# Optimization experiments

Hardware: AMD Instinct MI355X
Metric: run time of the kernel (lower is better)

The kernel has to match this reference:

```python
import jax, jax.numpy as jnp
import numpy as np

N = 50000
E = 800000
IN_DIM = 256
HID_DIM = 256
OUT_DIM = 128


def _gcn(x, src, dst, W, b):
    # PyG GCNConv: h = W x; add self-loops; sym-normalized scatter-add; + bias
    h = x @ W  # [N, out]
    deg = jax.ops.segment_sum(jnp.ones_like(dst, dtype=h.dtype), dst, num_segments=N)
    dinv = jax.lax.rsqrt(jnp.maximum(deg, 1e-12))
    norm = dinv[src] * dinv[dst]  # [E+N]
    msg = h[src] * norm[:, None]  # gather + scale
    out = jax.ops.segment_sum(msg, dst, num_segments=N)  # scatter-add
    return out + b


def _with_self_loops(edge):
    loops = jnp.arange(N, dtype=edge.dtype)
    src = jnp.concatenate([edge[0], loops])
    dst = jnp.concatenate([edge[1], loops])
    return src, dst


def setup_inputs() -> dict:
    key = jax.random.key(0)
    ks = jax.random.split(key, 20)
    d = {}
    d['x'] = jax.random.normal(ks[0], (N, IN_DIM), dtype=jnp.float32)
    d['edge_ppi'] = jax.random.randint(ks[1], (2, E), 0, N, dtype=jnp.int32)
    d['edge_path'] = jax.random.randint(ks[2], (2, E), 0, N, dtype=jnp.int32)
    d['edge_go'] = jax.random.randint(ks[3], (2, E), 0, N, dtype=jnp.int32)
    i = 4
    for name in ['ppi', 'path', 'go']:
        s1 = 1.0 / np.sqrt(IN_DIM)
        s2 = 1.0 / np.sqrt(HID_DIM)
        d[f'{name}_w1'] = jax.random.uniform(ks[i], (IN_DIM, HID_DIM), jnp.float32, -s1, s1); i += 1
        d[f'{name}_b1'] = jnp.zeros((HID_DIM,), jnp.float32)
        d[f'{name}_w2'] = jax.random.uniform(ks[i], (HID_DIM, OUT_DIM), jnp.float32, -s2, s2); i += 1
        d[f'{name}_b2'] = jnp.zeros((OUT_DIM,), jnp.float32)
    sa = 1.0 / np.sqrt(OUT_DIM)
    d['attn_w'] = jax.random.uniform(ks[i], (OUT_DIM, 1), jnp.float32, -sa, sa)
    d['attn_b'] = jnp.zeros((1,), jnp.float32)
    return d


def reference(x, edge_ppi, edge_path, edge_go,
              ppi_w1, ppi_b1, ppi_w2, ppi_b2,
              path_w1, path_b1, path_w2, path_b2,
              go_w1, go_b1, go_w2, go_b2,
              attn_w, attn_b):
    feats = []
    for edge, w1, b1, w2, b2 in [
        (edge_ppi, ppi_w1, ppi_b1, ppi_w2, ppi_b2),
        (edge_path, path_w1, path_b1, path_w2, path_b2),
        (edge_go, go_w1, go_b1, go_w2, go_b2),
    ]:
        src, dst = _with_self_loops(edge)
        h = jax.nn.relu(_gcn(x, src, dst, w1, b1))
        feats.append(_gcn(h, src, dst, w2, b2))
    all_feat = jnp.stack(feats, axis=1)  # [N, 3, out]
    attn = jax.nn.softmax(all_feat @ attn_w + attn_b, axis=1)  # [N, 3, 1]
    return jnp.sum(all_feat * attn, axis=1)  # [N, out]
```

## Files before the change

### kernel.cpp

```cpp
#include <hip/hip_runtime.h>

#define NN 50000
#define NE 800000
#define BINS 98
#define CAP 12288
#define EPB 4096
#define P1B ((NE + EPB - 1) / EPB)

typedef __attribute__((ext_vector_type(8))) short short8;
typedef __attribute__((ext_vector_type(4))) float f32x4;
typedef __attribute__((ext_vector_type(8))) unsigned short ushort8v;
typedef __attribute__((ext_vector_type(4))) unsigned short ushort4v;
typedef _Float16 half8 __attribute__((ext_vector_type(8)));

__device__ __forceinline__ ushort f2h(float f) {
    _Float16 h = (_Float16)f;
    return __builtin_bit_cast(ushort, h);
}
__device__ __forceinline__ float h2f(ushort u) {
    return (float)__builtin_bit_cast(_Float16, u);
}


__global__ __launch_bounds__(256) void k_bin(const int* __restrict__ e0,
                                             const int* __restrict__ e1,
                                             const int* __restrict__ e2,
                                             int* __restrict__ g_cur,
                                             unsigned* __restrict__ g_bins) {
    const int br = blockIdx.x / P1B;
    const int cb = blockIdx.x % P1B;
    const int* ep = (br == 0 ? e0 : br == 1 ? e1 : e2);
    const int tid = threadIdx.x;
    const int e_base = cb * EPB;

    __shared__ int s_cnt[BINS];
    __shared__ int s_start[BINS];
    __shared__ int s_cur[BINS];
    __shared__ int s_gb[BINS];
    __shared__ unsigned s_stage[EPB];

    if (tid < BINS) s_cnt[tid] = 0;
    __syncthreads();

    int4 s4[4], d4[4];
    bool valid[4];
#pragma unroll
    for (int i = 0; i < 4; ++i) {
        int idx = e_base + i * 1024 + tid * 4;
        valid[i] = (idx < NE);
        if (valid[i]) {
            s4[i] = *(const int4*)&ep[idx];
            d4[i] = *(const int4*)&ep[NE + idx];
            atomicAdd(&s_cnt[d4[i].x >> 9], 1);
            atomicAdd(&s_cnt[d4[i].y >> 9], 1);
            atomicAdd(&s_cnt[d4[i].z >> 9], 1);
            atomicAdd(&s_cnt[d4[i].w >> 9], 1);
        }
    }
    __syncthreads();
    if (tid == 0) {
        int run = 0;
        for (int b = 0; b < BINS; ++b) {
            s_start[b] = run;
            run += s_cnt[b];
        }
    }
    __syncthreads();
    if (tid < BINS) {
        s_cur[tid] = s_start[tid];
        int c = s_cnt[tid];
        int pc = (c + 15) & ~15;
        s_gb[tid] = (c > 0) ? atomicAdd(&g_cur[br * BINS + tid], pc) : 0;
    }
    __syncthreads();

#pragma unroll
    for (int i = 0; i < 4; ++i) {
        if (valid[i]) {
            int ss[4] = {s4[i].x, s4[i].y, s4[i].z, s4[i].w};
            int dd[4] = {d4[i].x, d4[i].y, d4[i].z, d4[i].w};
#pragma unroll
            for (int q = 0; q < 4; ++q) {
                int bin = dd[q] >> 9;
                int pos = atomicAdd(&s_cur[bin], 1);
                s_stage[pos] = ((unsigned)(dd[q] & 511) << 16) | (unsigned)ss[q];
            }
        }
    }
    __syncthreads();

    for (int b = 0; b < BINS; ++b) {
        int c = s_cnt[b];
        if (c == 0) continue;
        int st = s_start[b];
        int gb = s_gb[b];
        int pc = (c + 15) & ~15;
        if (gb + pc > CAP) pc = (gb < CAP) ? (CAP - gb) : 0;
        size_t obase = (size_t)(br * BINS + b) * CAP + gb;
        for (int j = tid; j < pc; j += 256)
            g_bins[obase + j] = (j < c) ? s_stage[st + j] : 0x80000000u;
    }
}


__device__ __forceinline__ int wave_incl_scan(int v, int lane) {
#pragma unroll
    for (int d = 1; d < 64; d <<= 1) {
        int u = __shfl_up(v, d);
        if (lane >= d) v += u;
    }
    return v;
}

__global__ __launch_bounds__(256) void k_build(const unsigned* __restrict__ g_bins,
                                               const int* __restrict__ g_cur,
                                               ushort* __restrict__ g_csr,
                                               int* __restrict__ seg3,
                                               int* __restrict__ cnt3,
                                               float* __restrict__ dinv3) {
    const int bid = blockIdx.x;
    const int br = bid / BINS;
    const int b2 = bid % BINS;
    const size_t base = (size_t)bid * CAP;
    const int node0 = b2 << 9;
    const int tid = threadIdx.x;

    __shared__ int s_cnt[512];
    __shared__ int s_off[512];
    __shared__ int s_wsum[4];

    s_cnt[tid] = 0;
    s_cnt[tid + 256] = 0;
    __syncthreads();

    const int total = min(g_cur[bid], CAP);
    for (int j = tid; j < total; j += 256) {
        unsigned p = g_bins[base + j];
        if (!(p & 0x80000000u)) atomicAdd(&s_cnt[(p >> 16) & 0x1FF], 1);
    }
    __syncthreads();

    const int lane = tid & 63, w = tid >> 6;
    int c0 = s_cnt[2 * tid], c1 = s_cnt[2 * tid + 1];
    int c2 = c0 + c1;
    int incl = wave_incl_scan(c2, lane);
    if (lane == 63) s_wsum[w] = incl;
    __syncthreads();
    int wpre = 0;
    for (int i = 0; i < w; ++i) wpre += s_wsum[i];
    int ex = wpre + incl - c2;
    s_off[2 * tid] = ex;
    s_off[2 * tid + 1] = ex + c0;

#pragma unroll
    for (int q = 0; q < 2; ++q) {
        int local = 2 * tid + q;
        int node = node0 + local;
        if (node < NN) {
            int g = br * NN + node;
            int c = (q == 0) ? c0 : c1;
            seg3[g] = (int)base + s_off[local];
            cnt3[g] = c;
            dinv3[g] = rsqrtf((float)(c + 1));
        }
    }
    __syncthreads();
    s_cnt[2 * tid] = s_off[2 * tid];
    s_cnt[2 * tid + 1] = s_off[2 * tid + 1];
    __syncthreads();

    for (int j = tid; j < total; j += 256) {
        unsigned p = g_bins[base + j];
        if (!(p & 0x80000000u)) {
            int loc = (p >> 16) & 0x1FF;
            int pos = atomicAdd(&s_cnt[loc], 1);
            g_csr[base + pos] = (ushort)(p & 0xFFFFu);
        }
    }
}


__global__ __launch_bounds__(256) void k_conv_x16(const float* __restrict__ x,
                                                  ushort* __restrict__ x16) {
    const int wid = threadIdx.x >> 6, lane = threadIdx.x & 63;
    const int row = blockIdx.x * 4 + wid;
    if (row >= NN) return;
    float4 v = *(const float4*)&x[(size_t)row * 256 + lane * 4];
    ushort4 o;
    o.x = f2h(v.x); o.y = f2h(v.y); o.z = f2h(v.z); o.w = f2h(v.w);
    *(ushort4*)&x16[(size_t)row * 256 + lane * 4] = o;
}

__global__ __launch_bounds__(256) void k_conv_w1(const float* __restrict__ w0,
                                                 const float* __restrict__ w1,
                                                 const float* __restrict__ w2,
                                                 ushort* __restrict__ BT1all) {
    int idx = blockIdx.x * 256 + threadIdx.x;
    int b = idx >> 16, r = idx & 65535;
    int k = r >> 8, n = r & 255;
    const float* W = (b == 0 ? w0 : b == 1 ? w1 : w2);
    BT1all[(size_t)b * 65536 + (size_t)n * 256 + k] = f2h(W[r]);
}

__global__ __launch_bounds__(256) void k_conv_w2(const float* __restrict__ w0,
                                                 const float* __restrict__ w1,
                                                 const float* __restrict__ w2,
                                                 ushort* __restrict__ BT2all) {
    int idx = blockIdx.x * 256 + threadIdx.x;
    int b = idx >> 15, r = idx & 32767;
    int k = r >> 7, n = r & 127;
    const float* W = (b == 0 ? w0 : b == 1 ? w1 : w2);
    BT2all[(size_t)b * 32768 + (size_t)n * 256 + k] = f2h(W[r]);
}


template <int BM, int BN, int N, int KK, bool XSWZ>
__global__ __launch_bounds__((BM / 64) * (BN / 64) * 64) void k_gemm(
    const ushort* __restrict__ A, size_t aBatch,
    const ushort* __restrict__ BTall, int btBatch,
    const float* __restrict__ dinv3, ushort* __restrict__ Call, size_t cBatch) {
    constexpr int WGN = BN / 64, NW = (BM / 64) * WGN;
    constexpr int BK = 32;
    constexpr int MT = (NN + BM - 1) / BM, NT = N / BN, GB = MT * NT;
    constexpr int NSTEP = KK / BK;
    __shared__ ushort sA[2][BM * BK];
    __shared__ ushort sB[2][BN * BK];
    int kb, bid;
    if constexpr (XSWZ) {
        int q = blockIdx.x >> 3, r = blockIdx.x & 7;
        bid = (q / 3) * 8 + r;
        kb = q % 3;
        if (bid >= GB) return;
    } else {
        kb = blockIdx.x / GB;
        bid = blockIdx.x % GB;
    }
    const ushort* Ab = A + (size_t)kb * aBatch;
    const ushort* BT = BTall + (size_t)kb * btBatch;
    const float* dinv = dinv3 + (size_t)kb * NN;
    ushort* C = Call + (size_t)kb * cBatch;
    const int t = threadIdx.x, lane = t & 63, wid = t >> 6;
    const int wm = (wid / WGN) * 64, wn = (wid % WGN) * 64;
    const int bm = (bid / NT) * BM;
    const int bn = (bid % NT) * BN;

    f32x4 zero = {0.f, 0.f, 0.f, 0.f};
    f32x4 acc[4][4];
#pragma unroll
    for (int m = 0; m < 4; ++m)
#pragma unroll
        for (int n = 0; n < 4; ++n) acc[m][n] = zero;

    constexpr int A_ISS = (BM * BK * 2) / (NW * 1024);
    constexpr int B_ISS = (BN * BK * 2) / (NW * 1024);

    auto stage = [&](int buf, int kt) {
#pragma unroll
        for (int i = 0; i < A_ISS; ++i) {
            int off = (wid + i * NW) << 10;
            int la = off + lane * 16;
            int row = la >> 6;
            int slot = (la >> 4) & 3;
            int scol = (slot ^ (row & 3)) << 4;
            int grow = bm + row;
            if (grow > NN - 1) grow = NN - 1;
            const char* ga = (const char*)Ab + (size_t)grow * (KK * 2) + kt * 2 + scol;
            __builtin_amdgcn_global_load_lds(
                (__attribute__((address_space(1))) const void*)ga,
                (__attribute__((address_space(3))) void*)((char*)sA[buf] + off), 16, 0, 0);
        }
#pragma unroll
        for (int i = 0; i < B_ISS; ++i) {
            int off = (wid + i * NW) << 10;
            int la = off + lane * 16;
            int row = la >> 6;
            int slot = (la >> 4) & 3;
            int scol = (slot ^ (row & 3)) << 4;
            const char* ga = (const char*)BT + (size_t)(bn + row) * (KK * 2) + kt * 2 + scol;
            __builtin_amdgcn_global_load_lds(
                (__attribute__((address_space(1))) const void*)ga,
                (__attribute__((address_space(3))) void*)((char*)sB[buf] + off), 16, 0, 0);
        }
    };

    stage(0, 0);
    __syncthreads();

    int cur = 0;
    for (int ts = 0; ts < NSTEP; ++ts) {
        if (ts + 1 < NSTEP) stage(cur ^ 1, (ts + 1) * BK);

        const int s = lane >> 4;
        const int r0 = lane & 15;
        short8 af[4], bf[4];
#pragma unroll
        for (int m = 0; m < 4; ++m) {
            int row = wm + m * 16 + r0;
            af[m] = *(const short8*)((const char*)sA[cur] + row * 64 + ((s ^ (row & 3)) << 4));
        }
#pragma unroll
        for (int n = 0; n < 4; ++n) {
            int row = wn + n * 16 + r0;
            bf[n] = *(const short8*)((const char*)sB[cur] + row * 64 + ((s ^ (row & 3)) << 4));
        }
#pragma unroll
        for (int m = 0; m < 4; ++m)
#pragma unroll
            for (int n = 0; n < 4; ++n)
                acc[m][n] = __builtin_amdgcn_mfma_f32_16x16x32_f16(
                    __builtin_bit_cast(half8, af[m]), __builtin_bit_cast(half8, bf[n]),
                    acc[m][n], 0, 0, 0);
        __syncthreads();
        cur ^= 1;
    }

    const int cr0 = (lane >> 4) * 4;
    const int cc = lane & 15;
#pragma unroll
    for (int m = 0; m < 4; ++m) {
#pragma unroll
        for (int r = 0; r < 4; ++r) {
            int row = bm + wm + m * 16 + cr0 + r;
            if (row < NN) {
                float dv = dinv[row];
#pragma unroll
                for (int n = 0; n < 4; ++n)
                    C[(size_t)row * N + bn + wn + n * 16 + cc] = f2h(acc[m][n][r] * dv);
            }
        }
    }
}


#define UTOT (3 * 12500)

__global__ __launch_bounds__(256) void k_agg1(const ushort* __restrict__ hs16all,
                                              const int* __restrict__ seg3,
                                              const int* __restrict__ cnt3,
                                              const ushort* __restrict__ g_csr,
                                              const float* __restrict__ dinv3,
                                              const float* __restrict__ b1a,
                                              const float* __restrict__ b1b,
                                              const float* __restrict__ b1c,
                                              ushort* __restrict__ h1all) {
    const int x = blockIdx.x & 7, j = blockIdx.x >> 3;
    const int start = (x * UTOT) >> 3;
    const int end = ((x + 1) * UTOT) >> 3;
    const int u = start + j;
    if (u >= end) return;
    const int b = u / 12500;
    const int blk = u % 12500;

    const int wid = threadIdx.x >> 6;
    const int lane = threadIdx.x & 63;
    const int node = blk * 4 + wid;
    if (node >= NN) return;
    const int half = lane >> 5, l32 = lane & 31;
    const int g = b * NN + node;
    const ushort* hs = hs16all + (size_t)b * NN * 256;
    const ushort* csr = g_csr + seg3[g];
    const int len = cnt3[g] + 1;
    const size_t colb = (size_t)l32 * 8;

    float acc[8] = {0.f, 0.f, 0.f, 0.f, 0.f, 0.f, 0.f, 0.f};
    int i = half;
    for (; i + 6 < len; i += 8) {
        int s0 = (i == 0) ? node : (int)csr[i - 1];
        int s1 = (int)csr[i + 1];
        int s2 = (int)csr[i + 3];
        int s3 = (int)csr[i + 5];
        ushort8v v0 = *(const ushort8v*)&hs[(size_t)s0 * 256 + colb];
        ushort8v v1 = *(const ushort8v*)&hs[(size_t)s1 * 256 + colb];
        ushort8v v2 = *(const ushort8v*)&hs[(size_t)s2 * 256 + colb];
        ushort8v v3 = *(const ushort8v*)&hs[(size_t)s3 * 256 + colb];
#pragma unroll
        for (int jq = 0; jq < 8; ++jq)
            acc[jq] += (h2f(v0[jq]) + h2f(v1[jq])) + (h2f(v2[jq]) + h2f(v3[jq]));
    }
    for (; i < len; i += 2) {
        int s = (i == 0) ? node : (int)csr[i - 1];
        ushort8v v = *(const ushort8v*)&hs[(size_t)s * 256 + colb];
#pragma unroll
        for (int jq = 0; jq < 8; ++jq) acc[jq] += h2f(v[jq]);
    }
#pragma unroll
    for (int jq = 0; jq < 8; ++jq) acc[jq] += __shfl_xor(acc[jq], 32);

    if (half == 0) {
        const float* bias = (b == 0 ? b1a : b == 1 ? b1b : b1c);
        const float di = dinv3[g];
        ushort8v o;
#pragma unroll
        for (int jq = 0; jq < 8; ++jq) {
            float r = fmaxf(di * acc[jq] + bias[l32 * 8 + jq], 0.f);
            o[jq] = f2h(r);
        }
        *(ushort8v*)&h1all[((size_t)b * NN + node) * 256 + colb] = o;
    }
}


__global__ __launch_bounds__(256) void k_final(const ushort* __restrict__ hs2all,
                                               const int* __restrict__ seg3,
                                               const int* __restrict__ cnt3,
                                               const ushort* __restrict__ g_csr,
                                               const float* __restrict__ dinv3,
                                               const float* __restrict__ b2a,
                                               const float* __restrict__ b2b,
                                               const float* __restrict__ b2c,
                                               const float* __restrict__ attn_w,
                                               const float* __restrict__ attn_b,
                                               float* __restrict__ out) {
    const int wid = threadIdx.x >> 6;
    const int lane = threadIdx.x & 63;
    const int node = blockIdx.x * 4 + wid;
    if (node >= NN) return;
    const int half = lane >> 5, l32 = lane & 31;
    const size_t colb = (size_t)l32 * 4;

    float f[3][4];
#pragma unroll
    for (int b = 0; b < 3; ++b) {
        const int g = b * NN + node;
        const ushort* hs = hs2all + (size_t)b * NN * 128;
        const ushort* csr = g_csr + seg3[g];
        const int len = cnt3[g] + 1;
        float acc[4] = {0.f, 0.f, 0.f, 0.f};
        int i = half;
        for (; i + 6 < len; i += 8) {
            int s0 = (i == 0) ? node : (int)csr[i - 1];
            int s1 = (int)csr[i + 1];
            int s2 = (int)csr[i + 3];
            int s3 = (int)csr[i + 5];
            ushort4v v0 = *(const ushort4v*)&hs[(size_t)s0 * 128 + colb];
            ushort4v v1 = *(const ushort4v*)&hs[(size_t)s1 * 128 + colb];
            ushort4v v2 = *(const ushort4v*)&hs[(size_t)s2 * 128 + colb];
            ushort4v v3 = *(const ushort4v*)&hs[(size_t)s3 * 128 + colb];
#pragma unroll
            for (int j = 0; j < 4; ++j)
                acc[j] += (h2f(v0[j]) + h2f(v1[j])) + (h2f(v2[j]) + h2f(v3[j]));
        }
        for (; i < len; i += 2) {
            int s = (i == 0) ? node : (int)csr[i - 1];
            ushort4v v = *(const ushort4v*)&hs[(size_t)s * 128 + colb];
#pragma unroll
            for (int j = 0; j < 4; ++j) acc[j] += h2f(v[j]);
        }
#pragma unroll
        for (int j = 0; j < 4; ++j) acc[j] += __shfl_xor(acc[j], 32);
        const float* bias = (b == 0 ? b2a : b == 1 ? b2b : b2c);
        const float di = dinv3[g];
#pragma unroll
        for (int j = 0; j < 4; ++j) f[b][j] = di * acc[j] + bias[l32 * 4 + j];
    }

    float4 w = *(const float4*)&attn_w[l32 * 4];
    float s0 = f[0][0] * w.x + f[0][1] * w.y + f[0][2] * w.z + f[0][3] * w.w;
    float s1 = f[1][0] * w.x + f[1][1] * w.y + f[1][2] * w.z + f[1][3] * w.w;
    float s2 = f[2][0] * w.x + f[2][1] * w.y + f[2][2] * w.z + f[2][3] * w.w;
#pragma unroll
    for (int m = 16; m >= 1; m >>= 1) {
        s0 += __shfl_xor(s0, m);
        s1 += __shfl_xor(s1, m);
        s2 += __shfl_xor(s2, m);
    }
    float bb = attn_b[0];
    s0 += bb; s1 += bb; s2 += bb;
    float mx = fmaxf(s0, fmaxf(s1, s2));
    float e0 = expf(s0 - mx), e1 = expf(s1 - mx), e2 = expf(s2 - mx);
    float inv = 1.f / (e0 + e1 + e2);
    e0 *= inv; e1 *= inv; e2 *= inv;

    if (half == 0) {
        float4 o;
        o.x = f[0][0] * e0 + f[1][0] * e1 + f[2][0] * e2;
        o.y = f[0][1] * e0 + f[1][1] * e1 + f[2][1] * e2;
        o.z = f[0][2] * e0 + f[1][2] * e1 + f[2][2] * e2;
        o.w = f[0][3] * e0 + f[1][3] * e1 + f[2][3] * e2;
        *(float4*)&out[(size_t)node * 128 + colb] = o;
    }
}


extern "C" void kernel_launch(void* const* d_in, const int* in_sizes, int n_in,
                              void* d_out, int out_size, void* d_ws, size_t ws_size,
                              hipStream_t stream) {
    const float* x = (const float*)d_in[0];
    const int* e0 = (const int*)d_in[1];
    const int* e1 = (const int*)d_in[2];
    const int* e2 = (const int*)d_in[3];
    const float* attn_w = (const float*)d_in[16];
    const float* attn_b = (const float*)d_in[17];

    char* ws = (char*)d_ws;
    size_t off = 0;
    auto alloc = [&](size_t bytes) -> void* {
        void* p = ws + off;
        off += (bytes + 255) & ~(size_t)255;
        return p;
    };

    int* g_cur      = (int*)alloc(3 * BINS * 4);
    int* seg3       = (int*)alloc((size_t)3 * NN * 4);
    int* cnt3       = (int*)alloc((size_t)3 * NN * 4);
    float* dinv3    = (float*)alloc((size_t)3 * NN * 4);
    ushort* g_csr   = (ushort*)alloc((size_t)3 * BINS * CAP * 2);
    ushort* x16     = (ushort*)alloc((size_t)NN * 256 * 2);
    ushort* hs16all = (ushort*)alloc((size_t)3 * NN * 256 * 2);
    ushort* h1all   = (ushort*)alloc((size_t)3 * NN * 256 * 2);
    unsigned* g_bins = (unsigned*)h1all;
    ushort* hs2all  = (ushort*)alloc((size_t)3 * NN * 128 * 2);
    ushort* BT1all  = (ushort*)alloc((size_t)3 * 256 * 256 * 2);
    ushort* BT2all  = (ushort*)alloc((size_t)3 * 128 * 256 * 2);

    const int WB = (NN + 3) / 4;

    hipMemsetAsync(g_cur, 0, 3 * BINS * 4, stream);
    k_conv_x16<<<WB, 256, 0, stream>>>(x, x16);
    k_conv_w1<<<768, 256, 0, stream>>>((const float*)d_in[4], (const float*)d_in[8],
                                       (const float*)d_in[12], BT1all);
    k_conv_w2<<<384, 256, 0, stream>>>((const float*)d_in[6], (const float*)d_in[10],
                                       (const float*)d_in[14], BT2all);

    k_bin<<<3 * P1B, 256, 0, stream>>>(e0, e1, e2, g_cur, g_bins);
    k_build<<<3 * BINS, 256, 0, stream>>>(g_bins, g_cur, g_csr, seg3, cnt3, dinv3);

    k_gemm<128, 256, 256, 256, true><<<1176, 512, 0, stream>>>(
        x16, 0, BT1all, 65536, dinv3, hs16all, (size_t)NN * 256);
    k_agg1<<<8 * ((UTOT + 7) / 8), 256, 0, stream>>>(
        hs16all, seg3, cnt3, g_csr, dinv3,
        (const float*)d_in[5], (const float*)d_in[9], (const float*)d_in[13], h1all);

    k_gemm<128, 128, 128, 256, false><<<3 * 391, 256, 0, stream>>>(
        h1all, (size_t)NN * 256, BT2all, 32768, dinv3, hs2all, (size_t)NN * 128);

    k_final<<<WB, 256, 0, stream>>>(hs2all, seg3, cnt3, g_csr, dinv3,
                                    (const float*)d_in[7], (const float*)d_in[11],
                                    (const float*)d_in[15], attn_w, attn_b,
                                    (float*)d_out);
}
```

Baseline: 427.0 us.

## Merge setup kernels and co-schedule CSR build with layer-1 GEMM

Folds edge binning, x conversion and both weight conversions into one launch with block-range dispatch. CSR build and the first GEMM now share one launch, because the GEMM no longer needs dinv. The source-side dinv scaling moves from the GEMM epilogue into the layer-1 aggregation as a per-neighbour gather and multiply. This cuts kernel launches and lets independent work overlap, but the aggregation gains extra scalar loads per edge and the GEMM blocks carry the build kernel's shared memory.

```diff
diff --git a/kernel.cpp b/kernel.cpp
--- a/kernel.cpp
+++ b/kernel.cpp
@@ -6,6 +6,8 @@
 #define CAP 12288
 #define EPB 4096
 #define P1B ((NE + EPB - 1) / EPB)
+#define BINB (3 * P1B)
+#define WB ((NN + 3) / 4)
 
 typedef __attribute__((ext_vector_type(8))) short short8;
 typedef __attribute__((ext_vector_type(4))) float f32x4;
@@ -21,88 +23,6 @@
     return (float)__builtin_bit_cast(_Float16, u);
 }
 
-
-__global__ __launch_bounds__(256) void k_bin(const int* __restrict__ e0,
-                                             const int* __restrict__ e1,
-                                             const int* __restrict__ e2,
-                                             int* __restrict__ g_cur,
-                                             unsigned* __restrict__ g_bins) {
-    const int br = blockIdx.x / P1B;
-    const int cb = blockIdx.x % P1B;
-    const int* ep = (br == 0 ? e0 : br == 1 ? e1 : e2);
-    const int tid = threadIdx.x;
-    const int e_base = cb * EPB;
-
-    __shared__ int s_cnt[BINS];
-    __shared__ int s_start[BINS];
-    __shared__ int s_cur[BINS];
-    __shared__ int s_gb[BINS];
-    __shared__ unsigned s_stage[EPB];
-
-    if (tid < BINS) s_cnt[tid] = 0;
-    __syncthreads();
-
-    int4 s4[4], d4[4];
-    bool valid[4];
-#pragma unroll
-    for (int i = 0; i < 4; ++i) {
-        int idx = e_base + i * 1024 + tid * 4;
-        valid[i] = (idx < NE);
-        if (valid[i]) {
-            s4[i] = *(const int4*)&ep[idx];
-            d4[i] = *(const int4*)&ep[NE + idx];
-            atomicAdd(&s_cnt[d4[i].x >> 9], 1);
-            atomicAdd(&s_cnt[d4[i].y >> 9], 1);
-            atomicAdd(&s_cnt[d4[i].z >> 9], 1);
-            atomicAdd(&s_cnt[d4[i].w >> 9], 1);
-        }
-    }
-    __syncthreads();
-    if (tid == 0) {
-        int run = 0;
-        for (int b = 0; b < BINS; ++b) {
-            s_start[b] = run;
-            run += s_cnt[b];
-        }
-    }
-    __syncthreads();
-    if (tid < BINS) {
-        s_cur[tid] = s_start[tid];
-        int c = s_cnt[tid];
-        int pc = (c + 15) & ~15;
-        s_gb[tid] = (c > 0) ? atomicAdd(&g_cur[br * BINS + tid], pc) : 0;
-    }
-    __syncthreads();
-
-#pragma unroll
-    for (int i = 0; i < 4; ++i) {
-        if (valid[i]) {
-            int ss[4] = {s4[i].x, s4[i].y, s4[i].z, s4[i].w};
-            int dd[4] = {d4[i].x, d4[i].y, d4[i].z, d4[i].w};
-#pragma unroll
-            for (int q = 0; q < 4; ++q) {
-                int bin = dd[q] >> 9;
-                int pos = atomicAdd(&s_cur[bin], 1);
-                s_stage[pos] = ((unsigned)(dd[q] & 511) << 16) | (unsigned)ss[q];
-            }
-        }
-    }
-    __syncthreads();
-
-    for (int b = 0; b < BINS; ++b) {
-        int c = s_cnt[b];
-        if (c == 0) continue;
-        int st = s_start[b];
-        int gb = s_gb[b];
-        int pc = (c + 15) & ~15;
-        if (gb + pc > CAP) pc = (gb < CAP) ? (CAP - gb) : 0;
-        size_t obase = (size_t)(br * BINS + b) * CAP + gb;
-        for (int j = tid; j < pc; j += 256)
-            g_bins[obase + j] = (j < c) ? s_stage[st + j] : 0x80000000u;
-    }
-}
-
-
 __device__ __forceinline__ int wave_incl_scan(int v, int lane) {
 #pragma unroll
     for (int d = 1; d < 64; d <<= 1) {
@@ -112,137 +32,300 @@
     return v;
 }
 
-__global__ __launch_bounds__(256) void k_build(const unsigned* __restrict__ g_bins,
-                                               const int* __restrict__ g_cur,
-                                               ushort* __restrict__ g_csr,
-                                               int* __restrict__ seg3,
-                                               int* __restrict__ cnt3,
-                                               float* __restrict__ dinv3) {
-    const int bid = blockIdx.x;
-    const int br = bid / BINS;
-    const int b2 = bid % BINS;
-    const size_t base = (size_t)bid * CAP;
-    const int node0 = b2 << 9;
+
+__global__ __launch_bounds__(256) void k_setup(
+    const int* __restrict__ e0, const int* __restrict__ e1,
+    const int* __restrict__ e2, int* __restrict__ g_cur,
+    unsigned* __restrict__ g_bins,
+    const float* __restrict__ x, ushort* __restrict__ x16,
+    const float* __restrict__ w1a, const float* __restrict__ w1b,
+    const float* __restrict__ w1c, ushort* __restrict__ BT1all,
+    const float* __restrict__ w2a, const float* __restrict__ w2b,
+    const float* __restrict__ w2c, ushort* __restrict__ BT2all) {
     const int tid = threadIdx.x;
 
+    if (blockIdx.x < BINB) {
+        const int br = blockIdx.x / P1B;
+        const int cb = blockIdx.x % P1B;
+        const int* ep = (br == 0 ? e0 : br == 1 ? e1 : e2);
+        const int e_base = cb * EPB;
+
+        __shared__ int s_cnt[BINS];
+        __shared__ int s_start[BINS];
+        __shared__ int s_cur[BINS];
+        __shared__ int s_gb[BINS];
+        __shared__ unsigned s_stage[EPB];
+
+        if (tid < BINS) s_cnt[tid] = 0;
+        __syncthreads();
+
+        int4 s4[4], d4[4];
+        bool valid[4];
+#pragma unroll
+        for (int i = 0; i < 4; ++i) {
+            int idx = e_base + i * 1024 + tid * 4;
+            valid[i] = (idx < NE);
+            if (valid[i]) {
+                s4[i] = *(const int4*)&ep[idx];
+                d4[i] = *(const int4*)&ep[NE + idx];
+                atomicAdd(&s_cnt[d4[i].x >> 9], 1);
+                atomicAdd(&s_cnt[d4[i].y >> 9], 1);
+                atomicAdd(&s_cnt[d4[i].z >> 9], 1);
+                atomicAdd(&s_cnt[d4[i].w >> 9], 1);
+            }
+        }
+        __syncthreads();
+        if (tid == 0) {
+            int run = 0;
+            for (int b = 0; b < BINS; ++b) {
+                s_start[b] = run;
+                run += s_cnt[b];
+            }
+        }
+        __syncthreads();
+        if (tid < BINS) {
+            s_cur[tid] = s_start[tid];
+            int c = s_cnt[tid];
+            int pc = (c + 15) & ~15;
+            s_gb[tid] = (c > 0) ? atomicAdd(&g_cur[br * BINS + tid], pc) : 0;
+        }
+        __syncthreads();
+
+#pragma unroll
+        for (int i = 0; i < 4; ++i) {
+            if (valid[i]) {
+                int ss[4] = {s4[i].x, s4[i].y, s4[i].z, s4[i].w};
+                int dd[4] = {d4[i].x, d4[i].y, d4[i].z, d4[i].w};
+#pragma unroll
+                for (int q = 0; q < 4; ++q) {
+                    int bin = dd[q] >> 9;
+                    int pos = atomicAdd(&s_cur[bin], 1);
+                    s_stage[pos] = ((unsigned)(dd[q] & 511) << 16) | (unsigned)ss[q];
+                }
+            }
+        }
+        __syncthreads();
+
+        for (int b = 0; b < BINS; ++b) {
+            int c = s_cnt[b];
+            if (c == 0) continue;
+            int st = s_start[b];
+            int gb = s_gb[b];
+            int pc = (c + 15) & ~15;
+            if (gb + pc > CAP) pc = (gb < CAP) ? (CAP - gb) : 0;
+            size_t obase = (size_t)(br * BINS + b) * CAP + gb;
+            for (int j = tid; j < pc; j += 256)
+                g_bins[obase + j] = (j < c) ? s_stage[st + j] : 0x80000000u;
+        }
+        return;
+    }
+
+    int bb = blockIdx.x - BINB;
+    if (bb < WB) {
+        const int wid = tid >> 6, lane = tid & 63;
+        const int row = bb * 4 + wid;
+        if (row >= NN) return;
+        float4 v = *(const float4*)&x[(size_t)row * 256 + lane * 4];
+        ushort4 o;
+        o.x = f2h(v.x); o.y = f2h(v.y); o.z = f2h(v.z); o.w = f2h(v.w);
+        *(ushort4*)&x16[(size_t)row * 256 + lane * 4] = o;
+        return;
+    }
+    bb -= WB;
+    if (bb < 768) {
+        int idx = bb * 256 + tid;
+        int b = idx >> 16, r = idx & 65535;
+        int k = r >> 8, n = r & 255;
+        const float* W = (b == 0 ? w1a : b == 1 ? w1b : w1c);
+        BT1all[(size_t)b * 65536 + (size_t)n * 256 + k] = f2h(W[r]);
+        return;
+    }
+    bb -= 768;
+    {
+        int idx = bb * 256 + tid;
+        int b = idx >> 15, r = idx & 32767;
+        int k = r >> 7, n = r & 127;
+        const float* W = (b == 0 ? w2a : b == 1 ? w2b : w2c);
+        BT2all[(size_t)b * 32768 + (size_t)n * 256 + k] = f2h(W[r]);
+    }
+}
+
+
+#define BGB 391
+
+__global__ __launch_bounds__(512) void k_build_gemm1(
+    const unsigned* __restrict__ g_bins, const int* __restrict__ g_cur,
+    ushort* __restrict__ g_csr, int* __restrict__ seg3, int* __restrict__ cnt3,
+    float* __restrict__ dinv3,
+    const ushort* __restrict__ x16, const ushort* __restrict__ BT1all,
+    ushort* __restrict__ hs16all) {
+    __shared__ ushort sA[2][128 * 32];
+    __shared__ ushort sB[2][256 * 32];
     __shared__ int s_cnt[512];
-    __shared__ int s_off[512];
-    __shared__ int s_wsum[4];
-
-    s_cnt[tid] = 0;
-    s_cnt[tid + 256] = 0;
-    __syncthreads();
-
-    const int total = min(g_cur[bid], CAP);
-    for (int j = tid; j < total; j += 256) {
-        unsigned p = g_bins[base + j];
-        if (!(p & 0x80000000u)) atomicAdd(&s_cnt[(p >> 16) & 0x1FF], 1);
-    }
-    __syncthreads();
-
-    const int lane = tid & 63, w = tid >> 6;
-    int c0 = s_cnt[2 * tid], c1 = s_cnt[2 * tid + 1];
-    int c2 = c0 + c1;
-    int incl = wave_incl_scan(c2, lane);
-    if (lane == 63) s_wsum[w] = incl;
-    __syncthreads();
-    int wpre = 0;
-    for (int i = 0; i < w; ++i) wpre += s_wsum[i];
-    int ex = wpre + incl - c2;
-    s_off[2 * tid] = ex;
-    s_off[2 * tid + 1] = ex + c0;
-
-#pragma unroll
-    for (int q = 0; q < 2; ++q) {
-        int local = 2 * tid + q;
-        int node = node0 + local;
+    __shared__ int s_wsum[8];
+
+    const int t = threadIdx.x, lane = t & 63, wid = t >> 6;
+
+    if (blockIdx.x < 3 * BINS) {
+        const int bid = blockIdx.x;
+        const int br = bid / BINS;
+        const int b2 = bid % BINS;
+        const size_t base = (size_t)bid * CAP;
+        const int node0 = b2 << 9;
+
+        s_cnt[t] = 0;
+        __syncthreads();
+
+        const int total = min(g_cur[bid], CAP);
+        for (int j = t; j < total; j += 512) {
+            unsigned p = g_bins[base + j];
+            if (!(p & 0x80000000u)) atomicAdd(&s_cnt[(p >> 16) & 0x1FF], 1);
+        }
+        __syncthreads();
+
+        int c = s_cnt[t];
+        int incl = wave_incl_scan(c, lane);
+        if (lane == 63) s_wsum[wid] = incl;
+        __syncthreads();
+        int wpre = 0;
+        for (int i = 0; i < wid; ++i) wpre += s_wsum[i];
+        int ex = wpre + incl - c;
+
+        int node = node0 + t;
         if (node < NN) {
             int g = br * NN + node;
-            int c = (q == 0) ? c0 : c1;
-            seg3[g] = (int)base + s_off[local];
+            seg3[g] = (int)base + ex;
             cnt3[g] = c;
             dinv3[g] = rsqrtf((float)(c + 1));
         }
-    }
+        __syncthreads();
+        s_cnt[t] = ex;
+        __syncthreads();
+
+        for (int j = t; j < total; j += 512) {
+            unsigned p = g_bins[base + j];
+            if (!(p & 0x80000000u)) {
+                int loc = (p >> 16) & 0x1FF;
+                int pos = atomicAdd(&s_cnt[loc], 1);
+                g_csr[base + pos] = (ushort)(p & 0xFFFFu);
+            }
+        }
+        return;
+    }
+
+    constexpr int BM = 128, BN = 256, N = 256, KK = 256, BK = 32;
+    constexpr int NW = 8, WGN = 4, NSTEP = KK / BK;
+    const int sbid = blockIdx.x - 3 * BINS;
+    int q = sbid >> 3, r = sbid & 7;
+    int bid = (q / 3) * 8 + r;
+    int kb = q % 3;
+    if (bid >= BGB) return;
+
+    const ushort* BT = BT1all + (size_t)kb * 65536;
+    ushort* C = hs16all + (size_t)kb * NN * 256;
+    const int wm = (wid / WGN) * 64, wn = (wid % WGN) * 64;
+    const int bm = bid * BM;
+
+    f32x4 zero = {0.f, 0.f, 0.f, 0.f};
+    f32x4 acc[4][4];
+#pragma unroll
+    for (int m = 0; m < 4; ++m)
+#pragma unroll
+        for (int n = 0; n < 4; ++n) acc[m][n] = zero;
+
+    auto stage = [&](int buf, int kt) {
+        {
+            int off = wid << 10;
+            int la = off + lane * 16;
+            int row = la >> 6;
+            int slot = (la >> 4) & 3;
+            int scol = (slot ^ (row & 3)) << 4;
+            int grow = bm + row;
+            if (grow > NN - 1) grow = NN - 1;
+            const char* ga = (const char*)x16 + (size_t)grow * (KK * 2) + kt * 2 + scol;
+            __builtin_amdgcn_global_load_lds(
+                (__attribute__((address_space(1))) const void*)ga,
+                (__attribute__((address_space(3))) void*)((char*)sA[buf] + off), 16, 0, 0);
+        }
+#pragma unroll
+        for (int i = 0; i < 2; ++i) {
+            int off = (wid + i * NW) << 10;
+            int la = off + lane * 16;
+            int row = la >> 6;
+            int slot = (la >> 4) & 3;
+            int scol = (slot ^ (row & 3)) << 4;
+            const char* ga = (const char*)BT + (size_t)row * (KK * 2) + kt * 2 + scol;
+            __builtin_amdgcn_global_load_lds(
+                (__attribute__((address_space(1))) const void*)ga,
+                (__attribute__((address_space(3))) void*)((char*)sB[buf] + off), 16, 0, 0);
+        }
+    };
+
+    stage(0, 0);
     __syncthreads();
-    s_cnt[2 * tid] = s_off[2 * tid];
-    s_cnt[2 * tid + 1] = s_off[2 * tid + 1];
-    __syncthreads();
-
-    for (int j = tid; j < total; j += 256) {
-        unsigned p = g_bins[base + j];
-        if (!(p & 0x80000000u)) {
-            int loc = (p >> 16) & 0x1FF;
-            int pos = atomicAdd(&s_cnt[loc], 1);
-            g_csr[base + pos] = (ushort)(p & 0xFFFFu);
-        }
-    }
-}
-
-
-__global__ __launch_bounds__(256) void k_conv_x16(const float* __restrict__ x,
-                                                  ushort* __restrict__ x16) {
-    const int wid = threadIdx.x >> 6, lane = threadIdx.x & 63;
-    const int row = blockIdx.x * 4 + wid;
-    if (row >= NN) return;
-    float4 v = *(const float4*)&x[(size_t)row * 256 + lane * 4];
-    ushort4 o;
-    o.x = f2h(v.x); o.y = f2h(v.y); o.z = f2h(v.z); o.w = f2h(v.w);
-    *(ushort4*)&x16[(size_t)row * 256 + lane * 4] = o;
-}
-
-__global__ __launch_bounds__(256) void k_conv_w1(const float* __restrict__ w0,
-                                                 const float* __restrict__ w1,
-                                                 const float* __restrict__ w2,
-                                                 ushort* __restrict__ BT1all) {
-    int idx = blockIdx.x * 256 + threadIdx.x;
-    int b = idx >> 16, r = idx & 65535;
-    int k = r >> 8, n = r & 255;
-    const float* W = (b == 0 ? w0 : b == 1 ? w1 : w2);
-    BT1all[(size_t)b * 65536 + (size_t)n * 256 + k] = f2h(W[r]);
-}
-
-__global__ __launch_bounds__(256) void k_conv_w2(const float* __restrict__ w0,
-                                                 const float* __restrict__ w1,
-                                                 const float* __restrict__ w2,
-                                                 ushort* __restrict__ BT2all) {
-    int idx = blockIdx.x * 256 + threadIdx.x;
-    int b = idx >> 15, r = idx & 32767;
-    int k = r >> 7, n = r & 127;
-    const float* W = (b == 0 ? w0 : b == 1 ? w1 : w2);
-    BT2all[(size_t)b * 32768 + (size_t)n * 256 + k] = f2h(W[r]);
-}
-
-
-template <int BM, int BN, int N, int KK, bool XSWZ>
-__global__ __launch_bounds__((BM / 64) * (BN / 64) * 64) void k_gemm(
-    const ushort* __restrict__ A, size_t aBatch,
-    const ushort* __restrict__ BTall, int btBatch,
-    const float* __restrict__ dinv3, ushort* __restrict__ Call, size_t cBatch) {
-    constexpr int WGN = BN / 64, NW = (BM / 64) * WGN;
-    constexpr int BK = 32;
-    constexpr int MT = (NN + BM - 1) / BM, NT = N / BN, GB = MT * NT;
-    constexpr int NSTEP = KK / BK;
-    __shared__ ushort sA[2][BM * BK];
-    __shared__ ushort sB[2][BN * BK];
-    int kb, bid;
-    if constexpr (XSWZ) {
-        int q = blockIdx.x >> 3, r = blockIdx.x & 7;
-        bid = (q / 3) * 8 + r;
-        kb = q % 3;
-        if (bid >= GB) return;
-    } else {
-        kb = blockIdx.x / GB;
-        bid = blockIdx.x % GB;
-    }
-    const ushort* Ab = A + (size_t)kb * aBatch;
-    const ushort* BT = BTall + (size_t)kb * btBatch;
+
+    int cur = 0;
+    for (int ts = 0; ts < NSTEP; ++ts) {
+        if (ts + 1 < NSTEP) stage(cur ^ 1, (ts + 1) * BK);
+
+        const int s = lane >> 4;
+        const int r0 = lane & 15;
+        short8 af[4], bf[4];
+#pragma unroll
+        for (int m = 0; m < 4; ++m) {
+            int row = wm + m * 16 + r0;
+            af[m] = *(const short8*)((const char*)sA[cur] + row * 64 + ((s ^ (row & 3)) << 4));
+        }
+#pragma unroll
+        for (int n = 0; n < 4; ++n) {
+            int row = wn + n * 16 + r0;
+            bf[n] = *(const short8*)((const char*)sB[cur] + row * 64 + ((s ^ (row & 3)) << 4));
+        }
+#pragma unroll
+        for (int m = 0; m < 4; ++m)
+#pragma unroll
+            for (int n = 0; n < 4; ++n)
+                acc[m][n] = __builtin_amdgcn_mfma_f32_16x16x32_f16(
+                    __builtin_bit_cast(half8, af[m]), __builtin_bit_cast(half8, bf[n]),
+                    acc[m][n], 0, 0, 0);
+        __syncthreads();
+        cur ^= 1;
+    }
+
+    const int cr0 = (lane >> 4) * 4;
+    const int cc = lane & 15;
+#pragma unroll
+    for (int m = 0; m < 4; ++m) {
+#pragma unroll
+        for (int rg = 0; rg < 4; ++rg) {
+            int row = bm + wm + m * 16 + cr0 + rg;
+            if (row < NN) {
+#pragma unroll
+                for (int n = 0; n < 4; ++n)
+                    C[(size_t)row * N + wn + n * 16 + cc] = f2h(acc[m][n][rg]);
+            }
+        }
+    }
+}
+
+
+__global__ __launch_bounds__(256) void k_gemm2(
+    const ushort* __restrict__ h1all, const ushort* __restrict__ BT2all,
+    const float* __restrict__ dinv3, ushort* __restrict__ hs2all) {
+    constexpr int BM = 128, BN = 128, N = 128, KK = 256, BK = 32;
+    constexpr int NW = 4, WGN = 2, NSTEP = KK / BK;
+    constexpr int MT = (NN + BM - 1) / BM;
+    __shared__ ushort sA[2][BM * 32];
+    __shared__ ushort sB[2][BN * 32];
+    const int kb = blockIdx.x / MT;
+    const int bid = blockIdx.x % MT;
+    const ushort* Ab = h1all + (size_t)kb * NN * 256;
+    const ushort* BT = BT2all + (size_t)kb * 32768;
     const float* dinv = dinv3 + (size_t)kb * NN;
-    ushort* C = Call + (size_t)kb * cBatch;
+    ushort* C = hs2all + (size_t)kb * NN * 128;
     const int t = threadIdx.x, lane = t & 63, wid = t >> 6;
     const int wm = (wid / WGN) * 64, wn = (wid % WGN) * 64;
-    const int bm = (bid / NT) * BM;
-    const int bn = (bid % NT) * BN;
+    const int bm = bid * BM;
 
     f32x4 zero = {0.f, 0.f, 0.f, 0.f};
     f32x4 acc[4][4];
@@ -251,12 +334,9 @@
 #pragma unroll
         for (int n = 0; n < 4; ++n) acc[m][n] = zero;
 
-    constexpr int A_ISS = (BM * BK * 2) / (NW * 1024);
-    constexpr int B_ISS = (BN * BK * 2) / (NW * 1024);
-
     auto stage = [&](int buf, int kt) {
 #pragma unroll
-        for (int i = 0; i < A_ISS; ++i) {
+        for (int i = 0; i < 2; ++i) {
             int off = (wid + i * NW) << 10;
             int la = off + lane * 16;
             int row = la >> 6;
@@ -270,13 +350,13 @@
                 (__attribute__((address_space(3))) void*)((char*)sA[buf] + off), 16, 0, 0);
         }
 #pragma unroll
-        for (int i = 0; i < B_ISS; ++i) {
+        for (int i = 0; i < 2; ++i) {
             int off = (wid + i * NW) << 10;
             int la = off + lane * 16;
             int row = la >> 6;
             int slot = (la >> 4) & 3;
             int scol = (slot ^ (row & 3)) << 4;
-            const char* ga = (const char*)BT + (size_t)(bn + row) * (KK * 2) + kt * 2 + scol;
+            const char* ga = (const char*)BT + (size_t)row * (KK * 2) + kt * 2 + scol;
             __builtin_amdgcn_global_load_lds(
                 (__attribute__((address_space(1))) const void*)ga,
                 (__attribute__((address_space(3))) void*)((char*)sB[buf] + off), 16, 0, 0);
@@ -319,13 +399,13 @@
 #pragma unroll
     for (int m = 0; m < 4; ++m) {
 #pragma unroll
-        for (int r = 0; r < 4; ++r) {
-            int row = bm + wm + m * 16 + cr0 + r;
+        for (int rg = 0; rg < 4; ++rg) {
+            int row = bm + wm + m * 16 + cr0 + rg;
             if (row < NN) {
                 float dv = dinv[row];
 #pragma unroll
                 for (int n = 0; n < 4; ++n)
-                    C[(size_t)row * N + bn + wn + n * 16 + cc] = f2h(acc[m][n][r] * dv);
+                    C[(size_t)row * N + wn + n * 16 + cc] = f2h(acc[m][n][rg] * dv);
             }
         }
     }
@@ -358,6 +438,7 @@
     const int half = lane >> 5, l32 = lane & 31;
     const int g = b * NN + node;
     const ushort* hs = hs16all + (size_t)b * NN * 256;
+    const float* dv = dinv3 + (size_t)b * NN;
     const ushort* csr = g_csr + seg3[g];
     const int len = cnt3[g] + 1;
     const size_t colb = (size_t)l32 * 8;
@@ -369,26 +450,29 @@
         int s1 = (int)csr[i + 1];
         int s2 = (int)csr[i + 3];
         int s3 = (int)csr[i + 5];
+        float d0 = dv[s0], d1 = dv[s1], d2 = dv[s2], d3 = dv[s3];
         ushort8v v0 = *(const ushort8v*)&hs[(size_t)s0 * 256 + colb];
         ushort8v v1 = *(const ushort8v*)&hs[(size_t)s1 * 256 + colb];
         ushort8v v2 = *(const ushort8v*)&hs[(size_t)s2 * 256 + colb];
         ushort8v v3 = *(const ushort8v*)&hs[(size_t)s3 * 256 + colb];
 #pragma unroll
         for (int jq = 0; jq < 8; ++jq)
-            acc[jq] += (h2f(v0[jq]) + h2f(v1[jq])) + (h2f(v2[jq]) + h2f(v3[jq]));
+            acc[jq] += (d0 * h2f(v0[jq]) + d1 * h2f(v1[jq])) +
+                       (d2 * h2f(v2[jq]) + d3 * h2f(v3[jq]));
     }
     for (; i < len; i += 2) {
         int s = (i == 0) ? node : (int)csr[i - 1];
+        float d = dv[s];
         ushort8v v = *(const ushort8v*)&hs[(size_t)s * 256 + colb];
 #pragma unroll
-        for (int jq = 0; jq < 8; ++jq) acc[jq] += h2f(v[jq]);
+        for (int jq = 0; jq < 8; ++jq) acc[jq] += d * h2f(v[jq]);
     }
 #pragma unroll
     for (int jq = 0; jq < 8; ++jq) acc[jq] += __shfl_xor(acc[jq], 32);
 
     if (half == 0) {
         const float* bias = (b == 0 ? b1a : b == 1 ? b1b : b1c);
-        const float di = dinv3[g];
+        const float di = dv[node];
         ushort8v o;
 #pragma unroll
         for (int jq = 0; jq < 8; ++jq) {
@@ -513,26 +597,21 @@
     ushort* BT1all  = (ushort*)alloc((size_t)3 * 256 * 256 * 2);
     ushort* BT2all  = (ushort*)alloc((size_t)3 * 128 * 256 * 2);
 
-    const int WB = (NN + 3) / 4;
-
     hipMemsetAsync(g_cur, 0, 3 * BINS * 4, stream);
-    k_conv_x16<<<WB, 256, 0, stream>>>(x, x16);
-    k_conv_w1<<<768, 256, 0, stream>>>((const float*)d_in[4], (const float*)d_in[8],
-                                       (const float*)d_in[12], BT1all);
-    k_conv_w2<<<384, 256, 0, stream>>>((const float*)d_in[6], (const float*)d_in[10],
-                                       (const float*)d_in[14], BT2all);
-
-    k_bin<<<3 * P1B, 256, 0, stream>>>(e0, e1, e2, g_cur, g_bins);
-    k_build<<<3 * BINS, 256, 0, stream>>>(g_bins, g_cur, g_csr, seg3, cnt3, dinv3);
-
-    k_gemm<128, 256, 256, 256, true><<<1176, 512, 0, stream>>>(
-        x16, 0, BT1all, 65536, dinv3, hs16all, (size_t)NN * 256);
+
+    k_setup<<<BINB + WB + 768 + 384, 256, 0, stream>>>(
+        e0, e1, e2, g_cur, g_bins, x, x16,
+        (const float*)d_in[4], (const float*)d_in[8], (const float*)d_in[12], BT1all,
+        (const float*)d_in[6], (const float*)d_in[10], (const float*)d_in[14], BT2all);
+
+    k_build_gemm1<<<3 * BINS + 1176, 512, 0, stream>>>(
+        g_bins, g_cur, g_csr, seg3, cnt3, dinv3, x16, BT1all, hs16all);
+
     k_agg1<<<8 * ((UTOT + 7) / 8), 256, 0, stream>>>(
         hs16all, seg3, cnt3, g_csr, dinv3,
         (const float*)d_in[5], (const float*)d_in[9], (const float*)d_in[13], h1all);
 
-    k_gemm<128, 128, 128, 256, false><<<3 * 391, 256, 0, stream>>>(
-        h1all, (size_t)NN * 256, BT2all, 32768, dinv3, hs2all, (size_t)NN * 128);
+    k_gemm2<<<3 * 391, 256, 0, stream>>>(h1all, BT2all, dinv3, hs2all);
 
     k_final<<<WB, 256, 0, stream>>>(hs2all, seg3, cnt3, g_csr, dinv3,
                                     (const float*)d_in[7], (const float*)d_in[11],
```

Result: faster. 403.1 us (-5.6%).
